# Performance work log

Hardware: AMD Instinct MI355X
Metric: run time of the kernel (lower is better)

Reference implementation:

```python
import jax, jax.numpy as jnp
import numpy as np

N_LEVELS = 16
F_PER_LEVEL = 2
TABLE_SIZE = 1 << 15          # 2**log2_hashmap_size
BASE_RES = 16
FINEST_RES = 512
PER_LEVEL_SCALE = (FINEST_RES / BASE_RES) ** (1.0 / (N_LEVELS - 1))
RANGE = np.pi                  # spherical coords live in [-pi, pi]
HASH_PRIME = np.uint32(2654435761)  # tcnn 2D hash prime (dim0 prime is 1)


def coord2sph(v):
    # unit vector -> (theta, phi): theta = acos(z) in [0, pi], phi = atan2(y, x) in [-pi, pi]
    theta = jnp.arccos(jnp.clip(v[..., 2], -1.0, 1.0))
    phi = jnp.arctan2(v[..., 1], v[..., 0])
    return jnp.stack([theta, phi], axis=-1)


def _normalize(v, eps=1e-12):
    # torch F.normalize: v / max(||v||, eps)
    n = jnp.linalg.norm(v, axis=-1, keepdims=True)
    return v / jnp.maximum(n, eps)


def hash_grid_encode(x01, table):
    """Instant-NGP style 2D multires hash encoding.
    x01: [N, 2] in [0, 1]; table: [L, T, F]. Returns [N, L*F]."""
    res = jnp.floor(BASE_RES * PER_LEVEL_SCALE ** jnp.arange(N_LEVELS)).astype(jnp.float32)  # [L]
    offs = jnp.array([[0, 0], [0, 1], [1, 0], [1, 1]], dtype=jnp.uint32)  # 4 corners
    offs_f = offs.astype(jnp.float32)

    def level(table_l, r):
        pos = x01 * r                      # [N,2]
        p0 = jnp.floor(pos)
        frac = pos - p0                    # [N,2]
        c = p0.astype(jnp.uint32)[:, None, :] + offs[None]          # [N,4,2]
        idx = (c[..., 0] ^ (c[..., 1] * HASH_PRIME)) % jnp.uint32(TABLE_SIZE)  # [N,4]
        feats = table_l[idx]               # [N,4,F] irregular gather
        w = jnp.prod(jnp.where(offs_f[None] > 0, frac[:, None, :], 1.0 - frac[:, None, :]), axis=-1)  # [N,4]
        return jnp.einsum('nc,ncf->nf', w, feats)  # [N,F]

    out = jax.vmap(level, in_axes=(0, 0), out_axes=1)(table, res)  # [N,L,F]
    return out.reshape(x01.shape[0], N_LEVELS * F_PER_LEVEL)


def setup_inputs() -> dict:
    key = jax.random.key(0)
    k1, k2, k3 = jax.random.split(key, 3)
    x = jax.random.normal(k1, (1048576, 6), dtype=jnp.float32)
    table1 = jax.random.uniform(k2, (N_LEVELS, TABLE_SIZE, F_PER_LEVEL), jnp.float32, -1e-4, 1e-4)
    table2 = jax.random.uniform(k3, (N_LEVELS, TABLE_SIZE, F_PER_LEVEL), jnp.float32, -1e-4, 1e-4)
    return {"x": x, "table1": table1, "table2": table2}


def reference(x, table1, table2):
    origin = x[:, :3]
    d = _normalize(x[:, 3:] - origin)                    # ray direction
    sph_d = (coord2sph(d) + RANGE) / (2.0 * RANGE)       # -> [0,1]^2
    hash_dir = hash_grid_encode(sph_d, table1)           # [N, 32]
    vect = jnp.cross(d, jnp.cross(origin, d))            # perpendicular foot vector
    sph_v = (coord2sph(_normalize(vect)) + RANGE) / (2.0 * RANGE)
    hash_vect = hash_grid_encode(sph_v, table2)          # [N, 32]
    return jnp.concatenate([vect, hash_dir, hash_vect], axis=-1)  # [N, 67]
```

## Files before the change

kernel.cpp:

```cpp
#include <hip/hip_runtime.h>
#include <math.h>

#define HASH_PRIME 2654435761u
#define TMASK 32767u
#define NPB 128
#define HWORDS 35
#define HSTRIDE 68
#define CHUNK 131072

typedef float vf2 __attribute__((ext_vector_type(2)));
typedef float vf4 __attribute__((ext_vector_type(4)));
typedef unsigned vu2 __attribute__((ext_vector_type(2)));

__device__ __forceinline__ unsigned pack_bf16(float a, float b) {
    return (__float_as_uint(a) >> 16) | (__float_as_uint(b) & 0xffff0000u);
}
__device__ __forceinline__ float bf_lo(unsigned w) { return __uint_as_float(w << 16); }
__device__ __forceinline__ float bf_hi(unsigned w) { return __uint_as_float(w & 0xffff0000u); }

__global__ __launch_bounds__(256)
void prepass(const float* __restrict__ x,
             const float* __restrict__ t1, const float* __restrict__ t2,
             unsigned* __restrict__ cD, unsigned* __restrict__ cV,
             vf4* __restrict__ vect, unsigned* __restrict__ Tp,
             int n, int nbp)
{
    if ((int)blockIdx.x >= nbp) {
        const int tb = (int)blockIdx.x - nbp;
        const float* src = (tb < 16) ? (t1 + (size_t)tb * 65536)
                                     : (t2 + (size_t)(tb - 16) * 65536);
        const vf4* s4 = (const vf4*)src;
        vu2* dst = (vu2*)(Tp + (size_t)tb * 32768);
        #pragma unroll 8
        for (int j = 0; j < 64; ++j) {
            const int k = j * 256 + (int)threadIdx.x;
            vf4 e = s4[k];
            vu2 w; w.x = pack_bf16(e.x, e.y); w.y = pack_bf16(e.z, e.w);
            dst[k] = w;
        }
        return;
    }

    const int i = blockIdx.x * 256 + threadIdx.x;
    if (i >= n) return;
    const float* xi = x + (long long)i * 6;
    vf2 p0 = __builtin_nontemporal_load((const vf2*)(xi + 0));
    vf2 p1 = __builtin_nontemporal_load((const vf2*)(xi + 2));
    vf2 p2 = __builtin_nontemporal_load((const vf2*)(xi + 4));
    float ox = p0.x, oy = p0.y, oz = p1.x;
    float dx = p1.y - ox, dy = p2.x - oy, dz = p2.y - oz;

    float nd = sqrtf(dx * dx + dy * dy + dz * dz);
    float invd = 1.0f / fmaxf(nd, 1e-12f);
    dx *= invd; dy *= invd; dz *= invd;

    float th_d = acosf(fminf(fmaxf(dz, -1.f), 1.f));
    float ph_d = atan2f(dy, dx);
    float u_d = (th_d + 3.14159265358979323846f) / 6.28318530717958647692f;
    float v_d = (ph_d + 3.14159265358979323846f) / 6.28318530717958647692f;

    float cx = oy * dz - oz * dy;
    float cy = oz * dx - ox * dz;
    float cz = ox * dy - oy * dx;
    float vx = dy * cz - dz * cy;
    float vy = dz * cx - dx * cz;
    float vz = dx * cy - dy * cx;

    float nv = sqrtf(vx * vx + vy * vy + vz * vz);
    float invv = 1.0f / fmaxf(nv, 1e-12f);
    float wx = vx * invv, wy = vy * invv, wz = vz * invv;
    float th_v = acosf(fminf(fmaxf(wz, -1.f), 1.f));
    float ph_v = atan2f(wy, wx);
    float u_v = (th_v + 3.14159265358979323846f) / 6.28318530717958647692f;
    float v_v = (ph_v + 3.14159265358979323846f) / 6.28318530717958647692f;

    unsigned ud = (unsigned)fminf(fmaxf(u_d, 0.f) * 65536.f, 65535.f);
    unsigned vd = (unsigned)fminf(fmaxf(v_d, 0.f) * 65536.f, 65535.f);
    unsigned uv = (unsigned)fminf(fmaxf(u_v, 0.f) * 65536.f, 65535.f);
    unsigned vv_ = (unsigned)fminf(fmaxf(v_v, 0.f) * 65536.f, 65535.f);
    __builtin_nontemporal_store(ud | (vd << 16), &cD[i]);
    __builtin_nontemporal_store(uv | (vv_ << 16), &cV[i]);
    vf4 vo; vo.x = vx; vo.y = vy; vo.z = vz; vo.w = 0.f;
    __builtin_nontemporal_store(vo, &vect[i]);
}

__device__ __forceinline__ unsigned enc_point(const unsigned* __restrict__ tl,
                                              float rs, unsigned cw)
{
    float pu = (float)(cw & 0xffffu) * rs;
    float pv = (float)(cw >> 16) * rs;
    float fu = floorf(pu), fv = floorf(pv);
    float au = pu - fu, av = pv - fv;
    unsigned cu = (unsigned)fu, cv = (unsigned)fv;
    unsigned h0 = cv * HASH_PRIME;
    unsigned h1 = (cv + 1u) * HASH_PRIME;
    unsigned w00 = tl[(cu ^ h0) & TMASK];
    unsigned w01 = tl[(cu ^ h1) & TMASK];
    unsigned w10 = tl[((cu + 1u) ^ h0) & TMASK];
    unsigned w11 = tl[((cu + 1u) ^ h1) & TMASK];
    float a00 = (1.f - au) * (1.f - av);
    float a01 = (1.f - au) * av;
    float a10 = au * (1.f - av);
    float a11 = au * av;
    float o0 = a00 * bf_lo(w00) + a01 * bf_lo(w01) + a10 * bf_lo(w10) + a11 * bf_lo(w11);
    float o1 = a00 * bf_hi(w00) + a01 * bf_hi(w01) + a10 * bf_hi(w10) + a11 * bf_hi(w11);
    return pack_bf16(o0, o1);
}

template<bool FULL, bool PACKED>
__global__ __launch_bounds__(1024)
void stageA(const float* __restrict__ t1, const float* __restrict__ t2,
            const unsigned* __restrict__ Tp,
            const unsigned* __restrict__ cD, const unsigned* __restrict__ cV,
            unsigned* __restrict__ F, int n)
{
    __shared__ unsigned tl[32768];
    const int tb = blockIdx.y;
    const float resv[16] = {16.f, 20.f, 25.f, 32.f, 40.f, 50.f, 64.f, 80.f,
                            101.f, 128.f, 161.f, 203.f, 256.f, 322.f, 406.f, 512.f};
    const float rs = resv[tb & 15] * (1.f / 65536.f);

    if constexpr (PACKED) {
        const vf4* s4 = (const vf4*)(Tp + (size_t)tb * 32768);
        vf4* tl4 = (vf4*)tl;
        #pragma unroll
        for (int j = 0; j < 8; ++j) {
            const int k = j * 1024 + threadIdx.x;
            tl4[k] = s4[k];
        }
    } else {
        const float* src = (tb < 16) ? (t1 + (size_t)tb * 65536)
                                     : (t2 + (size_t)(tb - 16) * 65536);
        const vf4* src4 = (const vf4*)src;
        vu2* tl2 = (vu2*)tl;
        #pragma unroll
        for (int j = 0; j < 16; ++j) {
            const int k = j * 1024 + threadIdx.x;
            vf4 e = src4[k];
            vu2 w; w.x = pack_bf16(e.x, e.y); w.y = pack_bf16(e.z, e.w);
            tl2[k] = w;
        }
    }
    __syncthreads();

    const unsigned* cc = (tb < 16) ? cD : cV;
    unsigned* Fo = F + (size_t)tb * (size_t)n;
    const int ibase = blockIdx.x * CHUNK + threadIdx.x;

    if (FULL) {
        #pragma unroll 2
        for (int k = 0; k < CHUNK / 1024; k += 4) {
            const int i0 = ibase + (k + 0) * 1024;
            const int i1 = ibase + (k + 1) * 1024;
            const int i2 = ibase + (k + 2) * 1024;
            const int i3 = ibase + (k + 3) * 1024;
            unsigned c0 = cc[i0];
            unsigned c1 = cc[i1];
            unsigned c2 = cc[i2];
            unsigned c3 = cc[i3];
            unsigned r0 = enc_point(tl, rs, c0);
            unsigned r1 = enc_point(tl, rs, c1);
            unsigned r2 = enc_point(tl, rs, c2);
            unsigned r3 = enc_point(tl, rs, c3);
            Fo[i0] = r0;
            Fo[i1] = r1;
            Fo[i2] = r2;
            Fo[i3] = r3;
        }
    } else {
        #pragma unroll 4
        for (int k = 0; k < CHUNK / 1024; ++k) {
            const int i = ibase + k * 1024;
            if (i < n) {
                unsigned c = cc[i];
                Fo[i] = enc_point(tl, rs, c);
            }
        }
    }
}

__global__ __launch_bounds__(NPB)
void stageB(const unsigned* __restrict__ F, const vf4* __restrict__ vect,
            float* __restrict__ out, int n)
{
    __shared__ unsigned hlds[NPB * HWORDS];
    __shared__ float vlds[NPB * 4];
    const int tid = threadIdx.x;
    const long long blk_start = (long long)blockIdx.x * NPB;
    const long long i = blk_start + tid;
    if (i < (long long)n) {
        vf4 vv = vect[i];
        vlds[tid * 4 + 0] = vv.x;
        vlds[tid * 4 + 1] = vv.y;
        vlds[tid * 4 + 2] = vv.z;
        unsigned* hrow = &hlds[tid * HWORDS];
        #pragma unroll
        for (int c = 0; c < 32; ++c)
            hrow[c] = F[(size_t)c * (size_t)n + i];
    }
    __syncthreads();

    const int rows = (int)(((blk_start + NPB) <= (long long)n) ? NPB : (n - blk_start));
    if (rows <= 0) return;
    const long long base = blk_start * 67ll;
    const int total = rows * 67;
    const unsigned short* hs = (const unsigned short*)hlds;

    const int nq = total >> 2;
    vf4* out4 = (vf4*)(out + base);
    for (int k = tid; k < nq; k += NPB) {
        vf4 o;
        #pragma unroll
        for (int j = 0; j < 4; ++j) {
            const int e = 4 * k + j;
            const int r = e / 67;
            const int c = e - r * 67;
            float val;
            if (c < 3) val = vlds[r * 4 + c];
            else       val = __uint_as_float((unsigned)hs[r * (2 * HWORDS) + (c - 3)] << 16);
            o[j] = val;
        }
        __builtin_nontemporal_store(o, &out4[k]);
    }
    for (int e = (nq << 2) + tid; e < total; e += NPB) {
        const int r = e / 67;
        const int c = e - r * 67;
        float val = (c < 3) ? vlds[r * 4 + c]
                            : __uint_as_float((unsigned)hs[r * (2 * HWORDS) + (c - 3)] << 16);
        __builtin_nontemporal_store(val, &out[base + e]);
    }
}

__device__ __forceinline__ void enc_level_f32(const float* __restrict__ tbl,
                                              float u, float v, float r,
                                              float& o0, float& o1)
{
    float pu = u * r, pv = v * r;
    float fu = floorf(pu), fv = floorf(pv);
    float au = pu - fu, av = pv - fv;
    unsigned cu = (unsigned)fu, cv = (unsigned)fv;
    unsigned h0 = cv * HASH_PRIME;
    unsigned h1 = (cv + 1u) * HASH_PRIME;
    unsigned i00 = (cu ^ h0) & TMASK;
    unsigned i01 = (cu ^ h1) & TMASK;
    unsigned i10 = ((cu + 1u) ^ h0) & TMASK;
    unsigned i11 = ((cu + 1u) ^ h1) & TMASK;
    vf2 g00 = *(const vf2*)(tbl + 2u * i00);
    vf2 g01 = *(const vf2*)(tbl + 2u * i01);
    vf2 g10 = *(const vf2*)(tbl + 2u * i10);
    vf2 g11 = *(const vf2*)(tbl + 2u * i11);
    float w00 = (1.f - au) * (1.f - av);
    float w01 = (1.f - au) * av;
    float w10 = au * (1.f - av);
    float w11 = au * av;
    o0 = w00 * g00.x + w01 * g01.x + w10 * g10.x + w11 * g11.x;
    o1 = w00 * g00.y + w01 * g01.y + w10 * g10.y + w11 * g11.y;
}

__global__ __launch_bounds__(NPB)
void hashprif_fallback(const float* __restrict__ x,
                       const float* __restrict__ t1,
                       const float* __restrict__ t2,
                       float* __restrict__ out,
                       int n)
{
    __shared__ unsigned hlds[NPB * (HSTRIDE / 2)];
    __shared__ float vlds[NPB * 4];
    const float res[16] = {16.f, 20.f, 25.f, 32.f, 40.f, 50.f, 64.f, 80.f,
                           101.f, 128.f, 161.f, 203.f, 256.f, 322.f, 406.f, 512.f};
    const int tid = threadIdx.x;
    const long long i = (long long)blockIdx.x * NPB + tid;
    const bool valid = i < (long long)n;

    if (valid) {
        const float* xi = x + i * 6ll;
        vf2 p0 = __builtin_nontemporal_load((const vf2*)(xi + 0));
        vf2 p1 = __builtin_nontemporal_load((const vf2*)(xi + 2));
        vf2 p2 = __builtin_nontemporal_load((const vf2*)(xi + 4));
        float ox = p0.x, oy = p0.y, oz = p1.x;
        float dx = p1.y - ox, dy = p2.x - oy, dz = p2.y - oz;
        float nd = sqrtf(dx * dx + dy * dy + dz * dz);
        float invd = 1.0f / fmaxf(nd, 1e-12f);
        dx *= invd; dy *= invd; dz *= invd;
        float th_d = acosf(fminf(fmaxf(dz, -1.f), 1.f));
        float ph_d = atan2f(dy, dx);
        float u_d = (th_d + 3.14159265358979323846f) / 6.28318530717958647692f;
        float v_d = (ph_d + 3.14159265358979323846f) / 6.28318530717958647692f;
        float cx = oy * dz - oz * dy;
        float cy = oz * dx - ox * dz;
        float cz = ox * dy - oy * dx;
        float vx = dy * cz - dz * cy;
        float vy = dz * cx - dx * cz;
        float vz = dx * cy - dy * cx;
        float nv = sqrtf(vx * vx + vy * vy + vz * vz);
        float invv = 1.0f / fmaxf(nv, 1e-12f);
        float wx = vx * invv, wy = vy * invv, wz = vz * invv;
        float th_v = acosf(fminf(fmaxf(wz, -1.f), 1.f));
        float ph_v = atan2f(wy, wx);
        float u_v = (th_v + 3.14159265358979323846f) / 6.28318530717958647692f;
        float v_v = (ph_v + 3.14159265358979323846f) / 6.28318530717958647692f;
        vlds[tid * 4 + 0] = vx;
        vlds[tid * 4 + 1] = vy;
        vlds[tid * 4 + 2] = vz;
        unsigned* hrow = &hlds[tid * (HSTRIDE / 2)];
        #pragma unroll
        for (int l = 0; l < 16; ++l) {
            float f0, f1;
            enc_level_f32(t1 + (size_t)l * 65536, u_d, v_d, res[l], f0, f1);
            hrow[l] = pack_bf16(f0, f1);
        }
        #pragma unroll
        for (int l = 0; l < 16; ++l) {
            float g0, g1;
            enc_level_f32(t2 + (size_t)l * 65536, u_v, v_v, res[l], g0, g1);
            hrow[16 + l] = pack_bf16(g0, g1);
        }
    }
    __syncthreads();
    const long long blk_start = (long long)blockIdx.x * NPB;
    const int rows = (int)(((blk_start + NPB) <= (long long)n) ? NPB : (n - blk_start));
    if (rows <= 0) return;
    const long long base = blk_start * 67ll;
    const int total = rows * 67;
    const unsigned short* hs = (const unsigned short*)hlds;
    for (int k = tid; k < total; k += NPB) {
        const int r = k / 67;
        const int c = k - r * 67;
        float val;
        if (c < 3) val = vlds[r * 4 + c];
        else {
            unsigned hv = (unsigned)hs[r * HSTRIDE + (c - 3)];
            val = __uint_as_float(hv << 16);
        }
        __builtin_nontemporal_store(val, &out[base + k]);
    }
}

extern "C" void kernel_launch(void* const* d_in, const int* in_sizes, int n_in,
                              void* d_out, int out_size, void* d_ws, size_t ws_size,
                              hipStream_t stream) {
    const float* x  = (const float*)d_in[0];
    const float* t1 = (const float*)d_in[1];
    const float* t2 = (const float*)d_in[2];
    float* out = (float*)d_out;
    const int n = in_sizes[0] / 6;
    const size_t nn = (size_t)n;
    const size_t base_need = 152ull * nn;
    const size_t tp_bytes  = 32ull * 32768ull * 4ull;
    const size_t need_packed = base_need + tp_bytes;

    if (ws_size >= base_need) {
        unsigned* cD = (unsigned*)d_ws;
        unsigned* cV = cD + nn;
        vf4* vect = (vf4*)((char*)d_ws + 8ull * nn);
        unsigned* F = (unsigned*)((char*)d_ws + 24ull * nn);
        const bool packed = (ws_size >= need_packed);
        unsigned* Tp = packed ? (unsigned*)((char*)d_ws + base_need) : (unsigned*)nullptr;

        const int nbp = (n + 255) / 256;
        const int gpre = packed ? (nbp + 32) : nbp;
        hipLaunchKernelGGL(prepass, dim3(gpre), dim3(256), 0, stream,
                           x, t1, t2, cD, cV, vect, Tp, n, nbp);

        dim3 ga((n + CHUNK - 1) / CHUNK, 32);
        if (n % CHUNK == 0) {
            if (packed)
                hipLaunchKernelGGL(HIP_KERNEL_NAME(stageA<true, true>), ga, dim3(1024), 0, stream,
                                   t1, t2, Tp, cD, cV, F, n);
            else
                hipLaunchKernelGGL(HIP_KERNEL_NAME(stageA<true, false>), ga, dim3(1024), 0, stream,
                                   t1, t2, Tp, cD, cV, F, n);
        } else {
            if (packed)
                hipLaunchKernelGGL(HIP_KERNEL_NAME(stageA<false, true>), ga, dim3(1024), 0, stream,
                                   t1, t2, Tp, cD, cV, F, n);
            else
                hipLaunchKernelGGL(HIP_KERNEL_NAME(stageA<false, false>), ga, dim3(1024), 0, stream,
                                   t1, t2, Tp, cD, cV, F, n);
        }
        hipLaunchKernelGGL(stageB, dim3((n + NPB - 1) / NPB), dim3(NPB), 0, stream,
                           F, vect, out, n);
    } else {
        hipLaunchKernelGGL(hashprif_fallback, dim3((n + NPB - 1) / NPB), dim3(NPB), 0, stream,
                           x, t1, t2, out, n);
    }
}
```

Measured before the change: 159.4 us.

## Store stage-A features in blocked tiles so stage B reads contiguous chunks

Stage A now writes encoded features in a tiled layout: each 128-point block gets a contiguous 4096-word region holding 32 feature columns. A new stageB_t reads each tile with coalesced nontemporal 16-byte loads, replacing 32 strided column reads per point. The change also halves CHUNK and reorders blockIdx.y to interleave the two tables and run the finest levels first, to balance work and scheduling. The fallback stageB is simplified to scalar stores.

```diff
diff --git a/kernel.cpp b/kernel.cpp
--- a/kernel.cpp
+++ b/kernel.cpp
@@ -6,11 +6,12 @@
 #define NPB 128
 #define HWORDS 35
 #define HSTRIDE 68
-#define CHUNK 131072
+#define CHUNK 65536
 
 typedef float vf2 __attribute__((ext_vector_type(2)));
 typedef float vf4 __attribute__((ext_vector_type(4)));
 typedef unsigned vu2 __attribute__((ext_vector_type(2)));
+typedef unsigned vu4 __attribute__((ext_vector_type(4)));
 
 __device__ __forceinline__ unsigned pack_bf16(float a, float b) {
     return (__float_as_uint(a) >> 16) | (__float_as_uint(b) & 0xffff0000u);
@@ -115,7 +116,8 @@
             unsigned* __restrict__ F, int n)
 {
     __shared__ unsigned tl[32768];
-    const int tb = blockIdx.y;
+    const int y = blockIdx.y;
+    const int tb = (y & 1) * 16 + (15 - (y >> 1));
     const float resv[16] = {16.f, 20.f, 25.f, 32.f, 40.f, 50.f, 64.f, 80.f,
                             101.f, 128.f, 161.f, 203.f, 256.f, 322.f, 406.f, 512.f};
     const float rs = resv[tb & 15] * (1.f / 65536.f);
@@ -144,10 +146,10 @@
     __syncthreads();
 
     const unsigned* cc = (tb < 16) ? cD : cV;
-    unsigned* Fo = F + (size_t)tb * (size_t)n;
     const int ibase = blockIdx.x * CHUNK + threadIdx.x;
 
     if (FULL) {
+        const unsigned tb7 = (unsigned)tb << 7;
         #pragma unroll 2
         for (int k = 0; k < CHUNK / 1024; k += 4) {
             const int i0 = ibase + (k + 0) * 1024;
@@ -162,12 +164,13 @@
             unsigned r1 = enc_point(tl, rs, c1);
             unsigned r2 = enc_point(tl, rs, c2);
             unsigned r3 = enc_point(tl, rs, c3);
-            Fo[i0] = r0;
-            Fo[i1] = r1;
-            Fo[i2] = r2;
-            Fo[i3] = r3;
+            F[(((unsigned)i0 >> 7) << 12) + tb7 + ((unsigned)i0 & 127u)] = r0;
+            F[(((unsigned)i1 >> 7) << 12) + tb7 + ((unsigned)i1 & 127u)] = r1;
+            F[(((unsigned)i2 >> 7) << 12) + tb7 + ((unsigned)i2 & 127u)] = r2;
+            F[(((unsigned)i3 >> 7) << 12) + tb7 + ((unsigned)i3 & 127u)] = r3;
         }
     } else {
+        unsigned* Fo = F + (size_t)tb * (size_t)n;
         #pragma unroll 4
         for (int k = 0; k < CHUNK / 1024; ++k) {
             const int i = ibase + k * 1024;
@@ -176,6 +179,71 @@
                 Fo[i] = enc_point(tl, rs, c);
             }
         }
+    }
+}
+
+__global__ __launch_bounds__(NPB)
+void stageB_t(const unsigned* __restrict__ F, const vf4* __restrict__ vect,
+              float* __restrict__ out, int n)
+{
+    __shared__ __align__(16) unsigned hlds2[32 * 132];
+    __shared__ float vlds[NPB * 4];
+    const int tid = threadIdx.x;
+    const long long blk_start = (long long)blockIdx.x * NPB;
+    const long long i = blk_start + tid;
+    if (i < (long long)n) {
+        vf4 vv = __builtin_nontemporal_load(&vect[i]);
+        vlds[tid * 4 + 0] = vv.x;
+        vlds[tid * 4 + 1] = vv.y;
+        vlds[tid * 4 + 2] = vv.z;
+    }
+    {
+        const vu4* Ft = (const vu4*)(F + (size_t)blockIdx.x * 4096);
+        const int p0 = 4 * (tid & 31);
+        #pragma unroll
+        for (int j = 0; j < 8; ++j) {
+            vu4 w = __builtin_nontemporal_load(&Ft[tid + 128 * j]);
+            const int c = 4 * j + (tid >> 5);
+            *(vu4*)&hlds2[c * 132 + p0] = w;
+        }
+    }
+    __syncthreads();
+
+    const int rows = (int)(((blk_start + NPB) <= (long long)n) ? NPB : (n - blk_start));
+    if (rows <= 0) return;
+    const long long base = blk_start * 67ll;
+    const int total = rows * 67;
+    const unsigned short* hs = (const unsigned short*)hlds2;
+
+    const int nq = total >> 2;
+    vf4* out4 = (vf4*)(out + base);
+    for (int k = tid; k < nq; k += NPB) {
+        vf4 o;
+        #pragma unroll
+        for (int j = 0; j < 4; ++j) {
+            const int e = 4 * k + j;
+            const int r = e / 67;
+            const int c = e - r * 67;
+            float val;
+            if (c < 3) val = vlds[r * 4 + c];
+            else {
+                const int f = c - 3;
+                val = __uint_as_float((unsigned)hs[(f >> 1) * 264 + 2 * r + (f & 1)] << 16);
+            }
+            o[j] = val;
+        }
+        __builtin_nontemporal_store(o, &out4[k]);
+    }
+    for (int e = (nq << 2) + tid; e < total; e += NPB) {
+        const int r = e / 67;
+        const int c = e - r * 67;
+        float val;
+        if (c < 3) val = vlds[r * 4 + c];
+        else {
+            const int f = c - 3;
+            val = __uint_as_float((unsigned)hs[(f >> 1) * 264 + 2 * r + (f & 1)] << 16);
+        }
+        __builtin_nontemporal_store(val, &out[base + e]);
     }
 }
 
@@ -205,29 +273,13 @@
     const long long base = blk_start * 67ll;
     const int total = rows * 67;
     const unsigned short* hs = (const unsigned short*)hlds;
-
-    const int nq = total >> 2;
-    vf4* out4 = (vf4*)(out + base);
-    for (int k = tid; k < nq; k += NPB) {
-        vf4 o;
-        #pragma unroll
-        for (int j = 0; j < 4; ++j) {
-            const int e = 4 * k + j;
-            const int r = e / 67;
-            const int c = e - r * 67;
-            float val;
-            if (c < 3) val = vlds[r * 4 + c];
-            else       val = __uint_as_float((unsigned)hs[r * (2 * HWORDS) + (c - 3)] << 16);
-            o[j] = val;
-        }
-        __builtin_nontemporal_store(o, &out4[k]);
-    }
-    for (int e = (nq << 2) + tid; e < total; e += NPB) {
-        const int r = e / 67;
-        const int c = e - r * 67;
-        float val = (c < 3) ? vlds[r * 4 + c]
-                            : __uint_as_float((unsigned)hs[r * (2 * HWORDS) + (c - 3)] << 16);
-        __builtin_nontemporal_store(val, &out[base + e]);
+    for (int k = tid; k < total; k += NPB) {
+        const int r = k / 67;
+        const int c = k - r * 67;
+        float val;
+        if (c < 3) val = vlds[r * 4 + c];
+        else       val = __uint_as_float((unsigned)hs[r * (2 * HWORDS) + (c - 3)] << 16);
+        __builtin_nontemporal_store(val, &out[base + k]);
     }
 }
 
@@ -363,13 +415,16 @@
                            x, t1, t2, cD, cV, vect, Tp, n, nbp);
 
         dim3 ga((n + CHUNK - 1) / CHUNK, 32);
-        if (n % CHUNK == 0) {
+        const bool full = (n % CHUNK == 0);
+        if (full) {
             if (packed)
                 hipLaunchKernelGGL(HIP_KERNEL_NAME(stageA<true, true>), ga, dim3(1024), 0, stream,
                                    t1, t2, Tp, cD, cV, F, n);
             else
                 hipLaunchKernelGGL(HIP_KERNEL_NAME(stageA<true, false>), ga, dim3(1024), 0, stream,
                                    t1, t2, Tp, cD, cV, F, n);
+            hipLaunchKernelGGL(stageB_t, dim3((n + NPB - 1) / NPB), dim3(NPB), 0, stream,
+                               F, vect, out, n);
         } else {
             if (packed)
                 hipLaunchKernelGGL(HIP_KERNEL_NAME(stageA<false, true>), ga, dim3(1024), 0, stream,
@@ -377,9 +432,9 @@
             else
                 hipLaunchKernelGGL(HIP_KERNEL_NAME(stageA<false, false>), ga, dim3(1024), 0, stream,
                                    t1, t2, Tp, cD, cV, F, n);
-        }
-        hipLaunchKernelGGL(stageB, dim3((n + NPB - 1) / NPB), dim3(NPB), 0, stream,
-                           F, vect, out, n);
+            hipLaunchKernelGGL(stageB, dim3((n + NPB - 1) / NPB), dim3(NPB), 0, stream,
+                               F, vect, out, n);
+        }
     } else {
         hipLaunchKernelGGL(hashprif_fallback, dim3((n + NPB - 1) / NPB), dim3(NPB), 0, stream,
                            x, t1, t2, out, n);
```

Measured after the change: 174.0 us. 1.09x slower.
